# Kernel optimization log

Hardware: AMD Instinct MI355X
Metric: run time of the kernel (lower is better)

## Reference

```python
import jax, jax.numpy as jnp
import numpy as np

WIN = 3  # win_size from init


def setup_inputs() -> dict:
    key = jax.random.key(0)
    ks = jax.random.split(key, 7)
    B, H, W, d = 8, 128, 128, 128
    N = H * W
    s = d ** -0.5  # param init scale
    return {
        "x": jax.random.normal(ks[0], (B, N, d), dtype=jnp.float32),
        "Wq": jax.random.normal(ks[1], (d, d), dtype=jnp.float32) * s,
        "bq": jax.random.normal(ks[2], (d,), dtype=jnp.float32) * 0.01,
        "Wk": jax.random.normal(ks[3], (d, d), dtype=jnp.float32) * s,
        "bk": jax.random.normal(ks[4], (d,), dtype=jnp.float32) * 0.01,
        "Wv": jax.random.normal(ks[5], (d, d), dtype=jnp.float32) * s,
        "bv": jax.random.normal(ks[6], (d,), dtype=jnp.float32) * 0.01,
        "H": H,
        "W": W,
    }


def reference(x, Wq, bq, Wk, bk, Wv, bv, H, W):
    B, N, d = x.shape
    scale = d ** -0.5
    pad = WIN // 2

    q = (x @ Wq + bq).reshape(B, H, W, d)
    k = (x @ Wk + bk).reshape(B, H, W, d)
    v = (x @ Wv + bv).reshape(B, H, W, d)

    # zero-pad spatial dims (matches F.pad); padded neighbors get logit 0, not -inf
    k_pad = jnp.pad(k, ((0, 0), (pad, pad), (pad, pad), (0, 0)))
    v_pad = jnp.pad(v, ((0, 0), (pad, pad), (pad, pad), (0, 0)))

    scores_l, vs_l = [], []
    for dy in range(WIN):
        for dx in range(WIN):
            k_slice = k_pad[:, dy:dy + H, dx:dx + W]   # [B,H,W,d]
            v_slice = v_pad[:, dy:dy + H, dx:dx + W]
            scores_l.append(jnp.einsum("bhwd,bhwd->bhw", q, k_slice) * scale)
            vs_l.append(v_slice)

    scores = jnp.stack(scores_l, axis=-1)            # [B,H,W,9]
    prob = jax.nn.softmax(scores, axis=-1)           # [B,H,W,9]
    v_stk = jnp.stack(vs_l, axis=-1)                 # [B,H,W,d,9]
    out = jnp.einsum("bhwn,bhwdn->bhwd", prob, v_stk)
    return out.reshape(B, N, d)
```

## Files before the change

### kernel.cpp

```cpp
#include <hip/hip_runtime.h>
#include <stdint.h>

#define B_ 8
#define H_ 128
#define W_ 128
#define D_ 128
#define N_ (H_*W_)
#define M_ (B_*N_)

typedef __attribute__((ext_vector_type(8))) short short8;
typedef __attribute__((ext_vector_type(4))) float floatx4;

__device__ inline unsigned short f2bf(float f){
  union { float f; unsigned int i; } c; c.f = f;
  unsigned int x = c.i;
  x += 0x7FFF + ((x >> 16) & 1);
  return (unsigned short)(x >> 16);
}
__device__ inline float bflo(unsigned int u){
  union { unsigned int i; float f; } c; c.i = u << 16; return c.f;
}
__device__ inline float bfhi(unsigned int u){
  union { unsigned int i; float f; } c; c.i = u & 0xFFFF0000u; return c.f;
}

__global__ void wtrans_kernel(const float* __restrict__ Wq, const float* __restrict__ Wk,
                              const float* __restrict__ Wv, unsigned short* __restrict__ Wt){
  const float* src = blockIdx.x == 0 ? Wq : (blockIdx.x == 1 ? Wk : Wv);
  unsigned short* dst = Wt + blockIdx.x * (D_*D_);
  const int i = blockIdx.y * 256 + threadIdx.x;
  const int k = i >> 7, n = i & 127;
  dst[n*D_ + k] = f2bf(src[i]);
}

__global__ __launch_bounds__(256, 2) void qkv_gemm_kernel(
    const float* __restrict__ x, const unsigned short* __restrict__ Wt,
    const float* __restrict__ bq, const float* __restrict__ bk, const float* __restrict__ bv,
    unsigned short* __restrict__ Q, unsigned short* __restrict__ K, unsigned short* __restrict__ V)
{
  const int rowTile = blockIdx.x;

  __shared__ unsigned short lds[8192];

  const int t = threadIdx.x;
  const int wave = t >> 6, lane = t & 63;

  {
    const float* xrow = x + (size_t)rowTile * 64 * D_;
    #pragma unroll
    for (int p = 0; p < 4; ++p){
      int s = p*256 + t;
      int r = s >> 4, cp = s & 15, c = cp ^ (r & 7);
      const float* gp = xrow + r*D_ + c*8;
      float4 f0 = *(const float4*)gp;
      float4 f1 = *(const float4*)(gp + 4);
      uint4 pk;
      pk.x = (unsigned)f2bf(f0.x) | ((unsigned)f2bf(f0.y) << 16);
      pk.y = (unsigned)f2bf(f0.z) | ((unsigned)f2bf(f0.w) << 16);
      pk.z = (unsigned)f2bf(f1.x) | ((unsigned)f2bf(f1.y) << 16);
      pk.w = (unsigned)f2bf(f1.z) | ((unsigned)f2bf(f1.w) << 16);
      *(uint4*)&lds[s*8] = pk;
    }
  }
  __syncthreads();

  const int wm = (wave >> 1) * 32, wn = (wave & 1) * 64;
  const int m0 = lane & 15, quad = lane >> 4;

  short8 a[4][2];
  #pragma unroll
  for (int kk = 0; kk < 4; ++kk)
    #pragma unroll
    for (int i = 0; i < 2; ++i){
      int row = wm + i*16 + m0;
      int c = (kk*4 + quad) ^ (row & 7);
      a[kk][i] = *(const short8*)&lds[row*128 + c*8];
    }

  #pragma unroll
  for (int which = 0; which < 3; ++which){
    const unsigned short* Wsel = Wt + which * (D_*D_);

    floatx4 acc[4][2] = {};
    #pragma unroll
    for (int kk = 0; kk < 4; ++kk){
      short8 b[4];
      #pragma unroll
      for (int j = 0; j < 4; ++j){
        int n = wn + j*16 + m0;
        b[j] = *(const short8*)(Wsel + n*128 + kk*32 + quad*8);
      }
      #pragma unroll
      for (int j = 0; j < 4; ++j)
        #pragma unroll
        for (int i = 0; i < 2; ++i)
          acc[j][i] = __builtin_amdgcn_mfma_f32_16x16x32_bf16(b[j], a[kk][i], acc[j][i], 0, 0, 0);
    }

    {
      const float* bias = which == 0 ? bq : (which == 1 ? bk : bv);
      unsigned short* Out = which == 0 ? Q : (which == 1 ? K : V);
      unsigned short* Outp = Out + (size_t)rowTile * 64 * D_;
      #pragma unroll
      for (int j = 0; j < 4; ++j){
        const float4 bb = *(const float4*)&bias[wn + j*16 + quad*4];
        #pragma unroll
        for (int i = 0; i < 2; ++i){
          const int row = wm + i*16 + m0;
          uint2 pk;
          pk.x = (unsigned)f2bf(acc[j][i][0] + bb.x) | ((unsigned)f2bf(acc[j][i][1] + bb.y) << 16);
          pk.y = (unsigned)f2bf(acc[j][i][2] + bb.z) | ((unsigned)f2bf(acc[j][i][3] + bb.w) << 16);
          *(uint2*)(Outp + row*D_ + wn + j*16 + quad*4) = pk;
        }
      }
    }
  }
}

__global__ __launch_bounds__(256, 2) void attn_kernel(
    const unsigned short* __restrict__ Q, const unsigned short* __restrict__ K,
    const unsigned short* __restrict__ V, float* __restrict__ out)
{
  const int t = threadIdx.x;
  const int e8 = t & 7;
  const int pix = blockIdx.x * 32 + (t >> 3);
  const int w = pix & 127;
  const int h = (pix >> 7) & 127;
  const int bbase = pix & ~(N_ - 1);
  const float scale = 0.08838834764831845f;
  const int doff = e8 * 16;
  const size_t off = (size_t)pix * D_ + doff;

  int npix[9]; bool okm[9];
  #pragma unroll
  for (int i = 0; i < 9; ++i){
    const int dy = i/3 - 1, dx = i%3 - 1;
    const int hh = h + dy, ww = w + dx;
    okm[i] = ((unsigned)hh < 128u) && ((unsigned)ww < 128u);
    const int hc = min(max(hh, 0), 127);
    const int wc = min(max(ww, 0), 127);
    npix[i] = bbase + hc*W_ + wc;
  }

  uint4 qu0, qu1;
  {
    const unsigned short* qp = Q + off;
    qu0 = *(const uint4*)qp;
    qu1 = *(const uint4*)(qp + 8);
  }
  uint4 ku[9][2];
  #pragma unroll
  for (int i = 0; i < 9; ++i){
    const unsigned short* kp = K + (size_t)npix[i]*D_ + doff;
    ku[i][0] = *(const uint4*)kp;
    ku[i][1] = *(const uint4*)(kp + 8);
  }
  uint4 vu[9][2];
  #pragma unroll
  for (int i = 0; i < 9; ++i){
    const unsigned short* vp = V + (size_t)npix[i]*D_ + doff;
    vu[i][0] = *(const uint4*)vp;
    vu[i][1] = *(const uint4*)(vp + 8);
  }

  float q[16];
  {
    unsigned uu[8] = {qu0.x, qu0.y, qu0.z, qu0.w, qu1.x, qu1.y, qu1.z, qu1.w};
    #pragma unroll
    for (int e = 0; e < 8; ++e){
      q[e*2]     = bflo(uu[e]) * scale;
      q[e*2 + 1] = bfhi(uu[e]) * scale;
    }
  }

  float s[9];
  #pragma unroll
  for (int i = 0; i < 9; ++i){
    unsigned uu[8] = {ku[i][0].x, ku[i][0].y, ku[i][0].z, ku[i][0].w,
                      ku[i][1].x, ku[i][1].y, ku[i][1].z, ku[i][1].w};
    float acc = 0.f;
    #pragma unroll
    for (int e = 0; e < 8; ++e){
      acc += q[e*2]     * bflo(uu[e]);
      acc += q[e*2 + 1] * bfhi(uu[e]);
    }
    s[i] = okm[i] ? acc : 0.f;
  }
  #pragma unroll
  for (int i = 0; i < 9; ++i){
    s[i] += __shfl_xor(s[i], 1, 64);
    s[i] += __shfl_xor(s[i], 2, 64);
    s[i] += __shfl_xor(s[i], 4, 64);
  }

  float m = s[0];
  #pragma unroll
  for (int i = 1; i < 9; ++i) m = fmaxf(m, s[i]);
  float p[9]; float l = 0.f;
  #pragma unroll
  for (int i = 0; i < 9; ++i){ p[i] = __expf(s[i] - m); l += p[i]; }
  const float inv = 1.f / l;

  float o[16];
  #pragma unroll
  for (int d = 0; d < 16; ++d) o[d] = 0.f;
  #pragma unroll
  for (int i = 0; i < 9; ++i){
    const float pi = okm[i] ? p[i] * inv : 0.f;
    unsigned uu[8] = {vu[i][0].x, vu[i][0].y, vu[i][0].z, vu[i][0].w,
                      vu[i][1].x, vu[i][1].y, vu[i][1].z, vu[i][1].w};
    #pragma unroll
    for (int e = 0; e < 8; ++e){
      o[e*2]     += pi * bflo(uu[e]);
      o[e*2 + 1] += pi * bfhi(uu[e]);
    }
  }

  float* op = out + off;
  #pragma unroll
  for (int c = 0; c < 4; ++c){
    float4 v4 = make_float4(o[c*4], o[c*4+1], o[c*4+2], o[c*4+3]);
    *(float4*)(op + c*4) = v4;
  }
}

extern "C" void kernel_launch(void* const* d_in, const int* in_sizes, int n_in,
                              void* d_out, int out_size, void* d_ws, size_t ws_size,
                              hipStream_t stream)
{
  const float* x  = (const float*)d_in[0];
  const float* Wq = (const float*)d_in[1];
  const float* bq = (const float*)d_in[2];
  const float* Wk = (const float*)d_in[3];
  const float* bk = (const float*)d_in[4];
  const float* Wv = (const float*)d_in[5];
  const float* bv = (const float*)d_in[6];
  float* out = (float*)d_out;

  char* ws = (char*)d_ws;
  unsigned short* Wt = (unsigned short*)ws;
  unsigned short* Q  = (unsigned short*)(ws + (1<<17));
  unsigned short* K  = (unsigned short*)(ws + (1<<17) + (size_t)M_*D_*2);
  unsigned short* V  = (unsigned short*)(ws + (1<<17) + (size_t)2*M_*D_*2);

  hipLaunchKernelGGL(wtrans_kernel, dim3(3, 64), dim3(256), 0, stream, Wq, Wk, Wv, Wt);
  hipLaunchKernelGGL(qkv_gemm_kernel, dim3(M_/64), dim3(256), 0, stream,
                     x, Wt, bq, bk, bv, Q, K, V);
  hipLaunchKernelGGL(attn_kernel, dim3(M_/32), dim3(256), 0, stream, Q, K, V, out);
}
```

Baseline: 227.0 us.

## Split QKV GEMM per projection and stage weights in LDS via async loads

The QKV GEMM grid now has a dimension per projection (Q, K, V), so each block computes one 64x128 output tile instead of all three. The block's 128x128 bf16 weight matrix is staged into swizzled LDS with global_load_lds, and each wave loads its own x fragments straight from global memory into registers with bf16 conversion, no longer going through LDS. This triples the block count and removes the uncoalesced per-lane global weight reads, but each x tile is now read and converted three times.

After: 229.0 us. About the same (+0.9%).

```diff
diff --git a/kernel.cpp b/kernel.cpp
--- a/kernel.cpp
+++ b/kernel.cpp
@@ -10,6 +10,9 @@
 
 typedef __attribute__((ext_vector_type(8))) short short8;
 typedef __attribute__((ext_vector_type(4))) float floatx4;
+
+typedef const __attribute__((address_space(1))) void* gas_t;
+typedef __attribute__((address_space(3))) void* las_t;
 
 __device__ inline unsigned short f2bf(float f){
   union { float f; unsigned int i; } c; c.f = f;
@@ -38,80 +41,89 @@
     const float* __restrict__ bq, const float* __restrict__ bk, const float* __restrict__ bv,
     unsigned short* __restrict__ Q, unsigned short* __restrict__ K, unsigned short* __restrict__ V)
 {
-  const int rowTile = blockIdx.x;
-
-  __shared__ unsigned short lds[8192];
+  const int which = blockIdx.x;
+  const int rowTile = blockIdx.y;
+
+  __shared__ unsigned short lds[16384];
 
   const int t = threadIdx.x;
   const int wave = t >> 6, lane = t & 63;
-
-  {
-    const float* xrow = x + (size_t)rowTile * 64 * D_;
-    #pragma unroll
-    for (int p = 0; p < 4; ++p){
+  const int m0 = lane & 15, quad = lane >> 4;
+  const int wm = (wave >> 1) * 32, wn = (wave & 1) * 64;
+
+  {
+    const unsigned short* Wsel = Wt + which * (D_*D_);
+    #pragma unroll
+    for (int p = 0; p < 8; ++p){
       int s = p*256 + t;
-      int r = s >> 4, cp = s & 15, c = cp ^ (r & 7);
-      const float* gp = xrow + r*D_ + c*8;
-      float4 f0 = *(const float4*)gp;
-      float4 f1 = *(const float4*)(gp + 4);
-      uint4 pk;
-      pk.x = (unsigned)f2bf(f0.x) | ((unsigned)f2bf(f0.y) << 16);
-      pk.y = (unsigned)f2bf(f0.z) | ((unsigned)f2bf(f0.w) << 16);
-      pk.z = (unsigned)f2bf(f1.x) | ((unsigned)f2bf(f1.y) << 16);
-      pk.w = (unsigned)f2bf(f1.z) | ((unsigned)f2bf(f1.w) << 16);
-      *(uint4*)&lds[s*8] = pk;
-    }
+      int n = s >> 4, cp = s & 15, c = cp ^ (n & 7);
+      __builtin_amdgcn_global_load_lds((gas_t)(const void*)(Wsel + n*128 + c*8),
+                                       (las_t)(void*)((unsigned short*)lds + p*2048 + wave*512),
+                                       16, 0, 0);
+    }
+  }
+
+  short8 a[4][2];
+  {
+    const float* xbase = x + (size_t)(rowTile*64 + wm + m0) * D_ + quad*8;
+    float4 f[8][2];
+    #pragma unroll
+    for (int kk = 0; kk < 4; ++kk)
+      #pragma unroll
+      for (int i = 0; i < 2; ++i){
+        const float* gp = xbase + i*16*D_ + kk*32;
+        f[kk*2+i][0] = *(const float4*)gp;
+        f[kk*2+i][1] = *(const float4*)(gp + 4);
+      }
+    #pragma unroll
+    for (int kk = 0; kk < 4; ++kk)
+      #pragma unroll
+      for (int i = 0; i < 2; ++i){
+        short8 v;
+        v[0] = (short)f2bf(f[kk*2+i][0].x);
+        v[1] = (short)f2bf(f[kk*2+i][0].y);
+        v[2] = (short)f2bf(f[kk*2+i][0].z);
+        v[3] = (short)f2bf(f[kk*2+i][0].w);
+        v[4] = (short)f2bf(f[kk*2+i][1].x);
+        v[5] = (short)f2bf(f[kk*2+i][1].y);
+        v[6] = (short)f2bf(f[kk*2+i][1].z);
+        v[7] = (short)f2bf(f[kk*2+i][1].w);
+        a[kk][i] = v;
+      }
   }
   __syncthreads();
 
-  const int wm = (wave >> 1) * 32, wn = (wave & 1) * 64;
-  const int m0 = lane & 15, quad = lane >> 4;
-
-  short8 a[4][2];
-  #pragma unroll
-  for (int kk = 0; kk < 4; ++kk)
-    #pragma unroll
-    for (int i = 0; i < 2; ++i){
-      int row = wm + i*16 + m0;
-      int c = (kk*4 + quad) ^ (row & 7);
-      a[kk][i] = *(const short8*)&lds[row*128 + c*8];
-    }
-
-  #pragma unroll
-  for (int which = 0; which < 3; ++which){
-    const unsigned short* Wsel = Wt + which * (D_*D_);
-
-    floatx4 acc[4][2] = {};
-    #pragma unroll
-    for (int kk = 0; kk < 4; ++kk){
-      short8 b[4];
-      #pragma unroll
-      for (int j = 0; j < 4; ++j){
-        int n = wn + j*16 + m0;
-        b[j] = *(const short8*)(Wsel + n*128 + kk*32 + quad*8);
-      }
-      #pragma unroll
-      for (int j = 0; j < 4; ++j)
-        #pragma unroll
-        for (int i = 0; i < 2; ++i)
-          acc[j][i] = __builtin_amdgcn_mfma_f32_16x16x32_bf16(b[j], a[kk][i], acc[j][i], 0, 0, 0);
-    }
-
-    {
-      const float* bias = which == 0 ? bq : (which == 1 ? bk : bv);
-      unsigned short* Out = which == 0 ? Q : (which == 1 ? K : V);
-      unsigned short* Outp = Out + (size_t)rowTile * 64 * D_;
-      #pragma unroll
-      for (int j = 0; j < 4; ++j){
-        const float4 bb = *(const float4*)&bias[wn + j*16 + quad*4];
-        #pragma unroll
-        for (int i = 0; i < 2; ++i){
-          const int row = wm + i*16 + m0;
-          uint2 pk;
-          pk.x = (unsigned)f2bf(acc[j][i][0] + bb.x) | ((unsigned)f2bf(acc[j][i][1] + bb.y) << 16);
-          pk.y = (unsigned)f2bf(acc[j][i][2] + bb.z) | ((unsigned)f2bf(acc[j][i][3] + bb.w) << 16);
-          *(uint2*)(Outp + row*D_ + wn + j*16 + quad*4) = pk;
-        }
+  floatx4 acc[4][2] = {};
+  #pragma unroll
+  for (int kk = 0; kk < 4; ++kk){
+    short8 b[4];
+    #pragma unroll
+    for (int j = 0; j < 4; ++j){
+      int n = wn + j*16 + m0;
+      int c = (kk*4 + quad) ^ (n & 7);
+      b[j] = *(const short8*)&lds[n*128 + c*8];
+    }
+    #pragma unroll
+    for (int j = 0; j < 4; ++j)
+      #pragma unroll
+      for (int i = 0; i < 2; ++i)
+        acc[j][i] = __builtin_amdgcn_mfma_f32_16x16x32_bf16(b[j], a[kk][i], acc[j][i], 0, 0, 0);
+  }
+
+  {
+    const float* bias = which == 0 ? bq : (which == 1 ? bk : bv);
+    unsigned short* Out = which == 0 ? Q : (which == 1 ? K : V);
+    unsigned short* Outp = Out + (size_t)rowTile * 64 * D_;
+    #pragma unroll
+    for (int j = 0; j < 4; ++j){
+      const float4 bb = *(const float4*)&bias[wn + j*16 + quad*4];
+      #pragma unroll
+      for (int i = 0; i < 2; ++i){
+        const int row = wm + i*16 + m0;
+        uint2 pk;
+        pk.x = (unsigned)f2bf(acc[j][i][0] + bb.x) | ((unsigned)f2bf(acc[j][i][1] + bb.y) << 16);
+        pk.y = (unsigned)f2bf(acc[j][i][2] + bb.z) | ((unsigned)f2bf(acc[j][i][3] + bb.w) << 16);
+        *(uint2*)(Outp + row*D_ + wn + j*16 + quad*4) = pk;
       }
     }
   }
@@ -244,7 +256,7 @@
   unsigned short* V  = (unsigned short*)(ws + (1<<17) + (size_t)2*M_*D_*2);
 
   hipLaunchKernelGGL(wtrans_kernel, dim3(3, 64), dim3(256), 0, stream, Wq, Wk, Wv, Wt);
-  hipLaunchKernelGGL(qkv_gemm_kernel, dim3(M_/64), dim3(256), 0, stream,
+  hipLaunchKernelGGL(qkv_gemm_kernel, dim3(3, M_/64), dim3(256), 0, stream,
                      x, Wt, bq, bk, bv, Q, K, V);
   hipLaunchKernelGGL(attn_kernel, dim3(M_/32), dim3(256), 0, stream, Q, K, V, out);
 }
```
